# Performance work log

Hardware: AMD Instinct MI355X
Metric: run time of the kernel (lower is better)

The kernel has to match this reference:

```python
import jax, jax.numpy as jnp
import numpy as np

N = 50000   # nodes
E = 640000  # edges per outer layer
D = 128     # in_channels == num_hidden_channels
H = 4       # attention heads
C = D // H  # per-head dim = 32
BS = 1024   # batch_size for output slice
LN_EPS = 1e-12


def setup_inputs() -> dict:
    key = jax.random.key(0)
    ks = jax.random.split(key, 16)
    w = lambda k, shape: (jax.random.normal(k, shape, dtype=jnp.float32) * 0.05)
    return {
        "embs": jax.random.normal(ks[0], (N, D), dtype=jnp.float32),
        # GATv2 conv 0 (shared lin_l == lin_r since share_weights=True)
        "w0": w(ks[1], (D, H * C)),
        "b0": w(ks[2], (H * C,)),
        "att0": w(ks[3], (H, C)),
        "bias0": w(ks[4], (H * C,)),
        # GATv2 conv 1
        "w1": w(ks[5], (D, H * C)),
        "b1": w(ks[6], (H * C,)),
        "att1": w(ks[7], (H, C)),
        "bias1": w(ks[8], (H * C,)),
        # output head: Linear(D, D) + LayerNorm(D)
        "wout": w(ks[9], (D, D)),
        "bout": w(ks[10], (D,)),
        "gamma": jnp.ones((D,), dtype=jnp.float32),
        "beta": jnp.zeros((D,), dtype=jnp.float32),
        # graph structure (row 0 = source j, row 1 = target i, PyG convention)
        "edge_index0": jax.random.randint(ks[11], (2, E), 0, N, dtype=jnp.int32),
        "edge_index1": jax.random.randint(ks[12], (2, E), 0, N, dtype=jnp.int32),
        "batch_size": BS,
    }


def gatv2_conv(x, edge_index, w, b, att, bias):
    """PyG GATv2Conv: share_weights=True, add_self_loops=False, concat=True,
    negative_slope=0.2, edge_attr=None, eval mode (no attention dropout)."""
    xl = (x @ w + b).reshape(-1, H, C)          # [N, H, C]; x_l == x_r
    src, dst = edge_index[0], edge_index[1]
    xj = xl[src]                                # messages  [E, H, C]
    e = jax.nn.leaky_relu(xl[dst] + xj, negative_slope=0.2)
    alpha = jnp.einsum("ehc,hc->eh", e, att)    # [E, H]
    # segment softmax over incoming edges of each target node
    amax = jax.ops.segment_max(alpha, dst, num_segments=N)
    alpha = jnp.exp(alpha - amax[dst])
    denom = jax.ops.segment_sum(alpha, dst, num_segments=N)
    alpha = alpha / denom[dst]
    out = jax.ops.segment_sum(alpha[:, :, None] * xj, dst, num_segments=N)
    return out.reshape(-1, H * C) + bias        # [N, H*C]


def reference(embs, w0, b0, att0, bias0, w1, b1, att1, bias1,
              wout, bout, gamma, beta, edge_index0, edge_index1, batch_size):
    x = gatv2_conv(embs, edge_index0, w0, b0, att0, bias0)
    x = jax.nn.gelu(x, approximate=False)       # nn.GELU default (dropout is eval no-op)
    x = gatv2_conv(x, edge_index1, w1, b1, att1, bias1)
    # layernorm_output head on first batch_size nodes
    y = x[:batch_size] @ wout + bout
    mu = jnp.mean(y, axis=-1, keepdims=True)
    var = jnp.mean(jnp.square(y - mu), axis=-1, keepdims=True)
    return (y - mu) * jax.lax.rsqrt(var + LN_EPS) * gamma + beta
```

## Files before the change

kernel.cpp:

```cpp
#include <hip/hip_runtime.h>
#include <math.h>

#define DD 128
#define SLOT 64

typedef short bf16x8 __attribute__((ext_vector_type(8)));
typedef float f32x4  __attribute__((ext_vector_type(4)));

__device__ __forceinline__ unsigned bf16rne(float f) {
    unsigned u = __float_as_uint(f);
    return (u + 0x7FFFu + ((u >> 16) & 1u)) >> 16;
}
__device__ __forceinline__ float2 bf2f(unsigned u) {
    float2 r;
    r.x = __uint_as_float(u << 16);
    r.y = __uint_as_float(u & 0xFFFF0000u);
    return r;
}
__device__ __forceinline__ float gelu1(float v) {
    return 0.5f * v * (1.f + erff(v * 0.70710678118654752f));
}

__global__ __launch_bounds__(256) void k_mark(const int* __restrict__ src1,
                                              const int* __restrict__ dst1,
                                              int E1, int BS,
                                              unsigned* __restrict__ mb,
                                              const float* __restrict__ w0,
                                              const float* __restrict__ w1,
                                              unsigned short* __restrict__ wp0,
                                              unsigned short* __restrict__ wp1) {
    int idx = blockIdx.x * 256 + threadIdx.x;
    if (idx < 2 * DD * DD) {
        const float* w = (idx < DD * DD) ? w0 : w1;
        unsigned short* wp = (idx < DD * DD) ? wp0 : wp1;
        int i = idx & (DD * DD - 1);
        int k = i >> 7, c = i & 127;
        int nt = c >> 4, ks = k >> 5;
        int lane = (c & 15) | (((k >> 3) & 3) << 4);
        wp[(((nt * 4 + ks) * 64) + lane) * 8 + (k & 7)] =
            (unsigned short)bf16rne(w[k * DD + c]);
    }
    int base = blockIdx.x * 1024 + threadIdx.x;
    #pragma unroll
    for (int j = 0; j < 4; ++j) {
        int e = base + j * 256;
        if (e < E1) {
            int d = dst1[e];
            if (d < BS) {
                int s = src1[e];
                atomicOr(&mb[s >> 5], 1u << (s & 31));
            }
        }
    }
    int g = blockIdx.x * 256 + threadIdx.x;
    if (g < BS) atomicOr(&mb[g >> 5], 1u << (g & 31));
}

__device__ __forceinline__ void mfma_linear_rows(
        const float* __restrict__ x, const unsigned short* __restrict__ wp,
        const float* __restrict__ b, unsigned* __restrict__ xl,
        int rIn, int rowValid, int rbaseOut, int nrowsOut, int apply_gelu) {
    int lane = threadIdx.x & 63;
    int c = lane & 15, g = lane >> 4;
    f32x4 acc[8];
    #pragma unroll
    for (int nt = 0; nt < 8; ++nt) {
        float bb = b[nt * 16 + c];
        acc[nt] = (f32x4){bb, bb, bb, bb};
    }
    const bf16x8* wv = (const bf16x8*)wp;
    for (int ks = 0; ks < 4; ++ks) {
        float xr[8];
        if (rowValid) {
            const float4* xp = (const float4*)&x[(size_t)rIn * DD + ks * 32 + g * 8];
            *(float4*)&xr[0] = xp[0];
            *(float4*)&xr[4] = xp[1];
            if (apply_gelu) {
                #pragma unroll
                for (int j = 0; j < 8; ++j) xr[j] = gelu1(xr[j]);
            }
        } else {
            #pragma unroll
            for (int j = 0; j < 8; ++j) xr[j] = 0.f;
        }
        union { unsigned u[4]; bf16x8 v; } af;
        #pragma unroll
        for (int j = 0; j < 4; ++j)
            af.u[j] = bf16rne(xr[2 * j]) | (bf16rne(xr[2 * j + 1]) << 16);
        #pragma unroll
        for (int nt = 0; nt < 8; ++nt) {
            bf16x8 bv = wv[(nt * 4 + ks) * 64 + lane];
            acc[nt] = __builtin_amdgcn_mfma_f32_16x16x32_bf16(af.v, bv, acc[nt], 0, 0, 0);
        }
    }
    int g4 = g * 4;
    #pragma unroll
    for (int nt = 0; nt < 8; ++nt) {
        #pragma unroll
        for (int reg = 0; reg < 4; ++reg) {
            unsigned u = bf16rne(acc[nt][reg]);
            unsigned up = (unsigned)__shfl_xor((int)u, 1, 64);
            int row = rbaseOut + g4 + reg;
            if (!(c & 1) && row < nrowsOut)
                xl[(size_t)row * 64 + (nt * 16 + c) / 2] = u | (up << 16);
        }
    }
}

__global__ __launch_bounds__(256) void k_hflin(
        const float* __restrict__ x, const unsigned short* __restrict__ wp,
        const float* __restrict__ b, unsigned* __restrict__ y, int nrows,
        int gLin, int gH0, int gH1,
        const int* __restrict__ src0, const int* __restrict__ dst0, int E0,
        const int* __restrict__ src1, const int* __restrict__ dst1, int E1,
        int BS, const unsigned* __restrict__ mb, int* __restrict__ cnt,
        int* __restrict__ ssrc, int N,
        int W, int* __restrict__ mex, int* __restrict__ mbsum) {
    if (blockIdx.x >= gLin) {
        int role = blockIdx.x - gLin;
        if (role < gH0) {
            int base = role * 1024 + threadIdx.x;
            #pragma unroll
            for (int j = 0; j < 4; ++j) {
                int e = base + j * 256;
                if (e < E0) {
                    int d = dst0[e];
                    if ((mb[d >> 5] >> (d & 31)) & 1u) {
                        int r = atomicAdd(&cnt[d], 1);
                        if (r < SLOT) ssrc[(size_t)d * SLOT + r] = src0[e];
                    }
                }
            }
        } else if (role < gH0 + gH1) {
            int base = (role - gH0) * 1024 + threadIdx.x;
            #pragma unroll
            for (int j = 0; j < 4; ++j) {
                int e = base + j * 256;
                if (e < E1) {
                    int d = dst1[e];
                    if (d < BS) {
                        int r = atomicAdd(&cnt[N + d], 1);
                        if (r < SLOT) ssrc[(size_t)(N + d) * SLOT + r] = src1[e];
                    }
                }
            }
        } else {
            __shared__ int s[256];
            int idx = (role - gH0 - gH1) * 256 + threadIdx.x;
            int v = (idx < W) ? __popc(mb[idx]) : 0;
            s[threadIdx.x] = v;
            __syncthreads();
            for (int o = 1; o < 256; o <<= 1) {
                int t = (threadIdx.x >= o) ? s[threadIdx.x - o] : 0;
                __syncthreads();
                s[threadIdx.x] += t;
                __syncthreads();
            }
            if (idx < W) mex[idx] = s[threadIdx.x] - v;
            if (threadIdx.x == 255) mbsum[role - gH0 - gH1] = s[255];
        }
        return;
    }
    int wave = threadIdx.x >> 6;
    int rb = blockIdx.x * 64 + wave * 16;
    int rIn = rb + ((threadIdx.x & 63) & 15);
    mfma_linear_rows(x, wp, b, y, rIn, rIn < nrows, rb, nrows, 0);
}

__global__ __launch_bounds__(256) void k_aggL(const unsigned* __restrict__ xl,
                                              const int* __restrict__ cnt,
                                              const int* __restrict__ ssrc,
                                              const float* __restrict__ att,
                                              const float* __restrict__ bias,
                                              float* __restrict__ out,
                                              const unsigned* __restrict__ mb,
                                              int n, int gMs, int W,
                                              const int* __restrict__ mex,
                                              const int* __restrict__ mbsum,
                                              int* __restrict__ livelist,
                                              int* __restrict__ nLive) {
    if (blockIdx.x < gMs) {
        int pre = 0;
        for (int i = 0; i < (int)blockIdx.x; ++i) pre += mbsum[i];
        int idx = blockIdx.x * 256 + threadIdx.x;
        if (idx < W) {
            unsigned word = mb[idx];
            int base = mex[idx] + pre;
            unsigned wt = word;
            while (wt) {
                int bit = __ffs(wt) - 1;
                livelist[base + __popc(word & ((1u << bit) - 1u))] = idx * 32 + bit;
                wt &= wt - 1;
            }
            if (idx == W - 1) *nLive = base + __popc(word);
        }
        return;
    }
    int node = __builtin_amdgcn_readfirstlane((blockIdx.x - gMs) * 4 +
                                              (threadIdx.x >> 6));
    if (node >= n) return;
    if (!((mb[node >> 5] >> (node & 31)) & 1u)) return;
    int lane = threadIdx.x & 63;
    float2 attv = *(const float2*)&att[lane * 2];
    float2 xd = bf2f(xl[(size_t)node * 64 + lane]);
    int rs  = node * SLOT;
    int deg = cnt[node];
    deg = deg > SLOT ? SLOT : deg;

    float m = -3.4e38f, den = 0.f, accx = 0.f, accy = 0.f;
    int sA = (deg > 0) ? ssrc[rs] : 0;
    int sB = (deg > 1) ? ssrc[rs + 1] : 0;
    unsigned uA = xl[(size_t)sA * 64 + lane];
    unsigned uB = xl[(size_t)sB * 64 + lane];

    int k = 0;
    for (; k + 1 < deg; k += 2) {
        int sC = (k + 2 < deg) ? ssrc[rs + k + 2] : 0;
        int sD = (k + 3 < deg) ? ssrc[rs + k + 3] : 0;
        unsigned uC = xl[(size_t)sC * 64 + lane];
        unsigned uD = xl[(size_t)sD * 64 + lane];
        float2 vA = bf2f(uA), vB = bf2f(uB);

        float tx = xd.x + vA.x, ty = xd.y + vA.y;
        tx = tx > 0.f ? tx : 0.2f * tx;
        ty = ty > 0.f ? ty : 0.2f * ty;
        float l0 = tx * attv.x + ty * attv.y;
        tx = xd.x + vB.x; ty = xd.y + vB.y;
        tx = tx > 0.f ? tx : 0.2f * tx;
        ty = ty > 0.f ? ty : 0.2f * ty;
        float l1 = tx * attv.x + ty * attv.y;
        #pragma unroll
        for (int o = 8; o; o >>= 1) {
            l0 += __shfl_xor(l0, o, 64);
            l1 += __shfl_xor(l1, o, 64);
        }
        float mn = fmaxf(fmaxf(m, l0), l1);
        float corr = __expf(m - mn);
        float w0 = __expf(l0 - mn);
        float w1 = __expf(l1 - mn);
        den  = den  * corr + w0 + w1;
        accx = accx * corr + w0 * vA.x + w1 * vB.x;
        accy = accy * corr + w0 * vA.y + w1 * vB.y;
        m = mn;
        sA = sC; sB = sD; uA = uC; uB = uD;
    }
    if (k < deg) {
        float2 vA = bf2f(uA);
        float tx = xd.x + vA.x, ty = xd.y + vA.y;
        tx = tx > 0.f ? tx : 0.2f * tx;
        ty = ty > 0.f ? ty : 0.2f * ty;
        float l0 = tx * attv.x + ty * attv.y;
        #pragma unroll
        for (int o = 8; o; o >>= 1) l0 += __shfl_xor(l0, o, 64);
        float mn = fmaxf(m, l0);
        float corr = __expf(m - mn);
        float w0 = __expf(l0 - mn);
        den  = den  * corr + w0;
        accx = accx * corr + w0 * vA.x;
        accy = accy * corr + w0 * vA.y;
    }

    float inv = (deg > 0) ? 1.f / den : 0.f;
    float2 o2;
    o2.x = accx * inv + bias[lane * 2];
    o2.y = accy * inv + bias[lane * 2 + 1];
    *(float2*)&out[(size_t)node * DD + lane * 2] = o2;
}

__global__ __launch_bounds__(256) void k_linC(const float* __restrict__ x,
                                              const unsigned short* __restrict__ wp,
                                              const float* __restrict__ b,
                                              unsigned* __restrict__ y,
                                              const int* __restrict__ livelist,
                                              const int* __restrict__ nLive) {
    int nL = *nLive;
    int wave = threadIdx.x >> 6;
    int lb = blockIdx.x * 64 + wave * 16;
    if (blockIdx.x * 64 >= nL) return;
    int lane = threadIdx.x & 63;
    int liIn = lb + (lane & 15);
    int rIn = (liIn < nL) ? livelist[liIn] : 0;

    int c = lane & 15, g = lane >> 4;
    f32x4 acc[8];
    #pragma unroll
    for (int nt = 0; nt < 8; ++nt) {
        float bb = b[nt * 16 + c];
        acc[nt] = (f32x4){bb, bb, bb, bb};
    }
    const bf16x8* wv = (const bf16x8*)wp;
    for (int ks = 0; ks < 4; ++ks) {
        float xr[8];
        if (liIn < nL) {
            const float4* xp = (const float4*)&x[(size_t)rIn * DD + ks * 32 + g * 8];
            *(float4*)&xr[0] = xp[0];
            *(float4*)&xr[4] = xp[1];
            #pragma unroll
            for (int j = 0; j < 8; ++j) xr[j] = gelu1(xr[j]);
        } else {
            #pragma unroll
            for (int j = 0; j < 8; ++j) xr[j] = 0.f;
        }
        union { unsigned u[4]; bf16x8 v; } af;
        #pragma unroll
        for (int j = 0; j < 4; ++j)
            af.u[j] = bf16rne(xr[2 * j]) | (bf16rne(xr[2 * j + 1]) << 16);
        #pragma unroll
        for (int nt = 0; nt < 8; ++nt) {
            bf16x8 bv = wv[(nt * 4 + ks) * 64 + lane];
            acc[nt] = __builtin_amdgcn_mfma_f32_16x16x32_bf16(af.v, bv, acc[nt], 0, 0, 0);
        }
    }
    int g4 = g * 4;
    #pragma unroll
    for (int reg = 0; reg < 4; ++reg) {
        int liOut = lb + g4 + reg;
        int row = (liOut < nL) ? livelist[liOut] : -1;
        #pragma unroll
        for (int nt = 0; nt < 8; ++nt) {
            unsigned u = bf16rne(acc[nt][reg]);
            unsigned up = (unsigned)__shfl_xor((int)u, 1, 64);
            if (!(c & 1) && row >= 0)
                y[(size_t)row * 64 + (nt * 16 + c) / 2] = u | (up << 16);
        }
    }
}

__global__ __launch_bounds__(256) void k_agg1head(
        const unsigned* __restrict__ xl,
        const int* __restrict__ cnt, const int* __restrict__ ssrc,
        const float* __restrict__ att, const float* __restrict__ bias,
        const float* __restrict__ wout, const float* __restrict__ bout,
        const float* __restrict__ gamma, const float* __restrict__ beta,
        float* __restrict__ yout, int N, int BS) {
    __shared__ float xrow[4][DD];
    int wid  = threadIdx.x >> 6;
    int lane = threadIdx.x & 63;
    int node = blockIdx.x * 4 + wid;
    if (node >= BS) return;
    float2 attv = *(const float2*)&att[lane * 2];
    float2 xd = bf2f(xl[(size_t)node * 64 + lane]);
    int key = N + node;
    int rs  = key * SLOT;
    int deg = cnt[key];
    deg = deg > SLOT ? SLOT : deg;

    float m = -3.4e38f, den = 0.f, accx = 0.f, accy = 0.f;
    int sA = (deg > 0) ? ssrc[rs] : 0;
    int sB = (deg > 1) ? ssrc[rs + 1] : 0;
    unsigned uA = xl[(size_t)sA * 64 + lane];
    unsigned uB = xl[(size_t)sB * 64 + lane];

    int k = 0;
    for (; k + 1 < deg; k += 2) {
        int sC = (k + 2 < deg) ? ssrc[rs + k + 2] : 0;
        int sD = (k + 3 < deg) ? ssrc[rs + k + 3] : 0;
        unsigned uC = xl[(size_t)sC * 64 + lane];
        unsigned uD = xl[(size_t)sD * 64 + lane];
        float2 vA = bf2f(uA), vB = bf2f(uB);
        float tx = xd.x + vA.x, ty = xd.y + vA.y;
        tx = tx > 0.f ? tx : 0.2f * tx;
        ty = ty > 0.f ? ty : 0.2f * ty;
        float l0 = tx * attv.x + ty * attv.y;
        tx = xd.x + vB.x; ty = xd.y + vB.y;
        tx = tx > 0.f ? tx : 0.2f * tx;
        ty = ty > 0.f ? ty : 0.2f * ty;
        float l1 = tx * attv.x + ty * attv.y;
        #pragma unroll
        for (int o = 8; o; o >>= 1) {
            l0 += __shfl_xor(l0, o, 64);
            l1 += __shfl_xor(l1, o, 64);
        }
        float mn = fmaxf(fmaxf(m, l0), l1);
        float corr = __expf(m - mn);
        float w0 = __expf(l0 - mn);
        float w1 = __expf(l1 - mn);
        den  = den  * corr + w0 + w1;
        accx = accx * corr + w0 * vA.x + w1 * vB.x;
        accy = accy * corr + w0 * vA.y + w1 * vB.y;
        m = mn;
        sA = sC; sB = sD; uA = uC; uB = uD;
    }
    if (k < deg) {
        float2 vA = bf2f(uA);
        float tx = xd.x + vA.x, ty = xd.y + vA.y;
        tx = tx > 0.f ? tx : 0.2f * tx;
        ty = ty > 0.f ? ty : 0.2f * ty;
        float l0 = tx * attv.x + ty * attv.y;
        #pragma unroll
        for (int o = 8; o; o >>= 1) l0 += __shfl_xor(l0, o, 64);
        float mn = fmaxf(m, l0);
        float corr = __expf(m - mn);
        float w0 = __expf(l0 - mn);
        den  = den  * corr + w0;
        accx = accx * corr + w0 * vA.x;
        accy = accy * corr + w0 * vA.y;
    }

    float inv = (deg > 0) ? 1.f / den : 0.f;
    float2 o2;
    o2.x = accx * inv + bias[lane * 2];
    o2.y = accy * inv + bias[lane * 2 + 1];

    xrow[wid][lane * 2]     = o2.x;
    xrow[wid][lane * 2 + 1] = o2.y;
    float2 acc2 = *(const float2*)&bout[lane * 2];
    __syncthreads();
    #pragma unroll 4
    for (int kk = 0; kk < DD; ++kk) {
        float xv = xrow[wid][kk];
        float2 wv2 = *(const float2*)&wout[(size_t)kk * DD + lane * 2];
        acc2.x += xv * wv2.x;
        acc2.y += xv * wv2.y;
    }
    float s = acc2.x + acc2.y;
    #pragma unroll
    for (int o = 32; o; o >>= 1) s += __shfl_xor(s, o, 64);
    float mean = s * (1.f / 128.f);
    float dx = acc2.x - mean, dy = acc2.y - mean;
    float s2 = dx * dx + dy * dy;
    #pragma unroll
    for (int o = 32; o; o >>= 1) s2 += __shfl_xor(s2, o, 64);
    float rstd = rsqrtf(s2 * (1.f / 128.f) + 1e-12f);
    float2 g2 = *(const float2*)&gamma[lane * 2];
    float2 b2 = *(const float2*)&beta[lane * 2];
    float2 yo;
    yo.x = dx * rstd * g2.x + b2.x;
    yo.y = dy * rstd * g2.y + b2.y;
    *(float2*)&yout[(size_t)node * DD + lane * 2] = yo;
}

extern "C" void kernel_launch(void* const* d_in, const int* in_sizes, int n_in,
                              void* d_out, int out_size, void* d_ws, size_t ws_size,
                              hipStream_t stream) {
    const float* embs  = (const float*)d_in[0];
    const float* w0    = (const float*)d_in[1];
    const float* b0    = (const float*)d_in[2];
    const float* att0  = (const float*)d_in[3];
    const float* bias0 = (const float*)d_in[4];
    const float* w1    = (const float*)d_in[5];
    const float* b1    = (const float*)d_in[6];
    const float* att1  = (const float*)d_in[7];
    const float* bias1 = (const float*)d_in[8];
    const float* wout  = (const float*)d_in[9];
    const float* bout  = (const float*)d_in[10];
    const float* gamma = (const float*)d_in[11];
    const float* beta  = (const float*)d_in[12];
    const int* ei0 = (const int*)d_in[13];
    const int* ei1 = (const int*)d_in[14];

    int N  = in_sizes[0] / DD;
    int E0 = in_sizes[13] / 2;
    int E1 = in_sizes[14] / 2;
    int BS = out_size / DD;
    int n2 = N + BS;
    int W  = (N + 31) / 32;

    unsigned* xl   = (unsigned*)d_ws;
    float* out     = (float*)(xl + (size_t)N * 64);
    int* ssrc      = (int*)(out + (size_t)N * DD);
    int* cnt       = ssrc + (size_t)n2 * SLOT;
    unsigned* mb   = (unsigned*)(cnt + n2);
    int* mex       = (int*)(mb + W + 32);
    int* mbsum     = mex + W;
    int* livelist  = mbsum + 32;
    int* nLive     = livelist + N;
    unsigned short* wp0 = (unsigned short*)
        (((uintptr_t)(nLive + 1) + 15) & ~(uintptr_t)15);
    unsigned short* wp1 = wp0 + DD * DD;

    int gH0  = (E0 + 1023) / 1024;
    int gH1  = (E1 + 1023) / 1024;
    int gLin = (N + 63) / 64;
    int gMs  = (W + 255) / 256;

    hipMemsetAsync(cnt, 0, ((size_t)n2 + W + 32) * sizeof(int), stream);
    k_mark<<<gH1, 256, 0, stream>>>(ei1, ei1 + E1, E1, BS, mb, w0, w1, wp0, wp1);
    k_hflin<<<gLin + gH0 + gH1 + gMs, 256, 0, stream>>>(
        embs, wp0, b0, xl, N, gLin, gH0, gH1,
        ei0, ei0 + E0, E0, ei1, ei1 + E1, E1, BS,
        mb, cnt, ssrc, N, W, mex, mbsum);
    k_aggL<<<gMs + (N + 3) / 4, 256, 0, stream>>>(
        xl, cnt, ssrc, att0, bias0, out, mb, N, gMs, W,
        mex, mbsum, livelist, nLive);
    k_linC<<<gLin, 256, 0, stream>>>(out, wp1, b1, xl, livelist, nLive);
    k_agg1head<<<(BS + 3) / 4, 256, 0, stream>>>(
        xl, cnt, ssrc, att1, bias1,
        wout, bout, gamma, beta, (float*)d_out, N, BS);
}
```

Baseline: 94.58 us.

## Build live-node list via atomics in mark pass and stage weights in LDS

Live nodes are now appended to a compact list during the marking pass, using the old value returned by atomicOr, and the layer-1 CSR bucketing moves into that same kernel. This removes the popcount prefix-scan and list compaction stages. The aggregation kernel now launches over the live list instead of testing every node against the bitmask. Both MFMA linear kernels copy the packed bf16 weights into shared memory once per block, and the memset is replaced by a small zeroing kernel. In exchange, the live-list order becomes nondeterministic and all threads contend on a single global atomic counter.

```diff
diff --git a/kernel.cpp b/kernel.cpp
--- a/kernel.cpp
+++ b/kernel.cpp
@@ -21,10 +21,19 @@
     return 0.5f * v * (1.f + erff(v * 0.70710678118654752f));
 }
 
+__global__ __launch_bounds__(256) void k_zero(int* __restrict__ p, int T) {
+    int stride = gridDim.x * 256;
+    for (int i = blockIdx.x * 256 + threadIdx.x; i < T; i += stride) p[i] = 0;
+}
+
 __global__ __launch_bounds__(256) void k_mark(const int* __restrict__ src1,
                                               const int* __restrict__ dst1,
                                               int E1, int BS,
                                               unsigned* __restrict__ mb,
+                                              int* __restrict__ livelist,
+                                              int* __restrict__ nLive,
+                                              int* __restrict__ cnt,
+                                              int* __restrict__ ssrc, int N,
                                               const float* __restrict__ w0,
                                               const float* __restrict__ w1,
                                               unsigned short* __restrict__ wp0,
@@ -48,37 +57,73 @@
             int d = dst1[e];
             if (d < BS) {
                 int s = src1[e];
-                atomicOr(&mb[s >> 5], 1u << (s & 31));
+                int r = atomicAdd(&cnt[N + d], 1);
+                if (r < SLOT) ssrc[(size_t)(N + d) * SLOT + r] = s;
+                unsigned old = atomicOr(&mb[s >> 5], 1u << (s & 31));
+                if (!((old >> (s & 31)) & 1u))
+                    livelist[atomicAdd(nLive, 1)] = s;
             }
         }
     }
     int g = blockIdx.x * 256 + threadIdx.x;
-    if (g < BS) atomicOr(&mb[g >> 5], 1u << (g & 31));
-}
-
-__device__ __forceinline__ void mfma_linear_rows(
+    if (g < BS) {
+        unsigned old = atomicOr(&mb[g >> 5], 1u << (g & 31));
+        if (!((old >> (g & 31)) & 1u))
+            livelist[atomicAdd(nLive, 1)] = g;
+    }
+}
+
+__global__ __launch_bounds__(256) void k_hflin(
         const float* __restrict__ x, const unsigned short* __restrict__ wp,
-        const float* __restrict__ b, unsigned* __restrict__ xl,
-        int rIn, int rowValid, int rbaseOut, int nrowsOut, int apply_gelu) {
+        const float* __restrict__ b, unsigned* __restrict__ y, int nrows,
+        int gLin,
+        const int* __restrict__ src0, const int* __restrict__ dst0, int E0,
+        const unsigned* __restrict__ mb, int* __restrict__ cnt,
+        int* __restrict__ ssrc) {
+    __shared__ bf16x8 wl[2048];
+
+    if (blockIdx.x >= gLin) {
+        int role = blockIdx.x - gLin;
+        int base = role * 1024 + threadIdx.x;
+        #pragma unroll
+        for (int j = 0; j < 4; ++j) {
+            int e = base + j * 256;
+            if (e < E0) {
+                int d = dst0[e];
+                if ((mb[d >> 5] >> (d & 31)) & 1u) {
+                    int r = atomicAdd(&cnt[d], 1);
+                    if (r < SLOT) ssrc[(size_t)d * SLOT + r] = src0[e];
+                }
+            }
+        }
+        return;
+    }
+
+    const bf16x8* wg = (const bf16x8*)wp;
+    #pragma unroll
+    for (int i = 0; i < 8; ++i)
+        wl[threadIdx.x + i * 256] = wg[threadIdx.x + i * 256];
+    __syncthreads();
+
+    int wave = threadIdx.x >> 6;
+    int rb = blockIdx.x * 64 + wave * 16;
     int lane = threadIdx.x & 63;
     int c = lane & 15, g = lane >> 4;
+    int rIn = rb + c;
+    int rowValid = rIn < nrows;
+
     f32x4 acc[8];
     #pragma unroll
     for (int nt = 0; nt < 8; ++nt) {
         float bb = b[nt * 16 + c];
         acc[nt] = (f32x4){bb, bb, bb, bb};
     }
-    const bf16x8* wv = (const bf16x8*)wp;
     for (int ks = 0; ks < 4; ++ks) {
         float xr[8];
         if (rowValid) {
             const float4* xp = (const float4*)&x[(size_t)rIn * DD + ks * 32 + g * 8];
             *(float4*)&xr[0] = xp[0];
             *(float4*)&xr[4] = xp[1];
-            if (apply_gelu) {
-                #pragma unroll
-                for (int j = 0; j < 8; ++j) xr[j] = gelu1(xr[j]);
-            }
         } else {
             #pragma unroll
             for (int j = 0; j < 8; ++j) xr[j] = 0.f;
@@ -89,7 +134,7 @@
             af.u[j] = bf16rne(xr[2 * j]) | (bf16rne(xr[2 * j + 1]) << 16);
         #pragma unroll
         for (int nt = 0; nt < 8; ++nt) {
-            bf16x8 bv = wv[(nt * 4 + ks) * 64 + lane];
+            bf16x8 bv = wl[(nt * 4 + ks) * 64 + lane];
             acc[nt] = __builtin_amdgcn_mfma_f32_16x16x32_bf16(af.v, bv, acc[nt], 0, 0, 0);
         }
     }
@@ -100,71 +145,11 @@
         for (int reg = 0; reg < 4; ++reg) {
             unsigned u = bf16rne(acc[nt][reg]);
             unsigned up = (unsigned)__shfl_xor((int)u, 1, 64);
-            int row = rbaseOut + g4 + reg;
-            if (!(c & 1) && row < nrowsOut)
-                xl[(size_t)row * 64 + (nt * 16 + c) / 2] = u | (up << 16);
-        }
-    }
-}
-
-__global__ __launch_bounds__(256) void k_hflin(
-        const float* __restrict__ x, const unsigned short* __restrict__ wp,
-        const float* __restrict__ b, unsigned* __restrict__ y, int nrows,
-        int gLin, int gH0, int gH1,
-        const int* __restrict__ src0, const int* __restrict__ dst0, int E0,
-        const int* __restrict__ src1, const int* __restrict__ dst1, int E1,
-        int BS, const unsigned* __restrict__ mb, int* __restrict__ cnt,
-        int* __restrict__ ssrc, int N,
-        int W, int* __restrict__ mex, int* __restrict__ mbsum) {
-    if (blockIdx.x >= gLin) {
-        int role = blockIdx.x - gLin;
-        if (role < gH0) {
-            int base = role * 1024 + threadIdx.x;
-            #pragma unroll
-            for (int j = 0; j < 4; ++j) {
-                int e = base + j * 256;
-                if (e < E0) {
-                    int d = dst0[e];
-                    if ((mb[d >> 5] >> (d & 31)) & 1u) {
-                        int r = atomicAdd(&cnt[d], 1);
-                        if (r < SLOT) ssrc[(size_t)d * SLOT + r] = src0[e];
-                    }
-                }
-            }
-        } else if (role < gH0 + gH1) {
-            int base = (role - gH0) * 1024 + threadIdx.x;
-            #pragma unroll
-            for (int j = 0; j < 4; ++j) {
-                int e = base + j * 256;
-                if (e < E1) {
-                    int d = dst1[e];
-                    if (d < BS) {
-                        int r = atomicAdd(&cnt[N + d], 1);
-                        if (r < SLOT) ssrc[(size_t)(N + d) * SLOT + r] = src1[e];
-                    }
-                }
-            }
-        } else {
-            __shared__ int s[256];
-            int idx = (role - gH0 - gH1) * 256 + threadIdx.x;
-            int v = (idx < W) ? __popc(mb[idx]) : 0;
-            s[threadIdx.x] = v;
-            __syncthreads();
-            for (int o = 1; o < 256; o <<= 1) {
-                int t = (threadIdx.x >= o) ? s[threadIdx.x - o] : 0;
-                __syncthreads();
-                s[threadIdx.x] += t;
-                __syncthreads();
-            }
-            if (idx < W) mex[idx] = s[threadIdx.x] - v;
-            if (threadIdx.x == 255) mbsum[role - gH0 - gH1] = s[255];
-        }
-        return;
-    }
-    int wave = threadIdx.x >> 6;
-    int rb = blockIdx.x * 64 + wave * 16;
-    int rIn = rb + ((threadIdx.x & 63) & 15);
-    mfma_linear_rows(x, wp, b, y, rIn, rIn < nrows, rb, nrows, 0);
+            int row = rb + g4 + reg;
+            if (!(c & 1) && row < nrows)
+                y[(size_t)row * 64 + (nt * 16 + c) / 2] = u | (up << 16);
+        }
+    }
 }
 
 __global__ __launch_bounds__(256) void k_aggL(const unsigned* __restrict__ xl,
@@ -173,33 +158,11 @@
                                               const float* __restrict__ att,
                                               const float* __restrict__ bias,
                                               float* __restrict__ out,
-                                              const unsigned* __restrict__ mb,
-                                              int n, int gMs, int W,
-                                              const int* __restrict__ mex,
-                                              const int* __restrict__ mbsum,
-                                              int* __restrict__ livelist,
-                                              int* __restrict__ nLive) {
-    if (blockIdx.x < gMs) {
-        int pre = 0;
-        for (int i = 0; i < (int)blockIdx.x; ++i) pre += mbsum[i];
-        int idx = blockIdx.x * 256 + threadIdx.x;
-        if (idx < W) {
-            unsigned word = mb[idx];
-            int base = mex[idx] + pre;
-            unsigned wt = word;
-            while (wt) {
-                int bit = __ffs(wt) - 1;
-                livelist[base + __popc(word & ((1u << bit) - 1u))] = idx * 32 + bit;
-                wt &= wt - 1;
-            }
-            if (idx == W - 1) *nLive = base + __popc(word);
-        }
-        return;
-    }
-    int node = __builtin_amdgcn_readfirstlane((blockIdx.x - gMs) * 4 +
-                                              (threadIdx.x >> 6));
-    if (node >= n) return;
-    if (!((mb[node >> 5] >> (node & 31)) & 1u)) return;
+                                              const int* __restrict__ livelist,
+                                              const int* __restrict__ nLive) {
+    int li = blockIdx.x * 4 + (threadIdx.x >> 6);
+    if (li >= *nLive) return;
+    int node = __builtin_amdgcn_readfirstlane(livelist[li]);
     int lane = threadIdx.x & 63;
     float2 attv = *(const float2*)&att[lane * 2];
     float2 xd = bf2f(xl[(size_t)node * 64 + lane]);
@@ -273,22 +236,29 @@
                                               unsigned* __restrict__ y,
                                               const int* __restrict__ livelist,
                                               const int* __restrict__ nLive) {
+    __shared__ bf16x8 wl[2048];
     int nL = *nLive;
+    if (blockIdx.x * 64 >= nL) return;
+
+    const bf16x8* wg = (const bf16x8*)wp;
+    #pragma unroll
+    for (int i = 0; i < 8; ++i)
+        wl[threadIdx.x + i * 256] = wg[threadIdx.x + i * 256];
+    __syncthreads();
+
     int wave = threadIdx.x >> 6;
     int lb = blockIdx.x * 64 + wave * 16;
-    if (blockIdx.x * 64 >= nL) return;
     int lane = threadIdx.x & 63;
-    int liIn = lb + (lane & 15);
+    int c = lane & 15, g = lane >> 4;
+    int liIn = lb + c;
     int rIn = (liIn < nL) ? livelist[liIn] : 0;
 
-    int c = lane & 15, g = lane >> 4;
     f32x4 acc[8];
     #pragma unroll
     for (int nt = 0; nt < 8; ++nt) {
         float bb = b[nt * 16 + c];
         acc[nt] = (f32x4){bb, bb, bb, bb};
     }
-    const bf16x8* wv = (const bf16x8*)wp;
     for (int ks = 0; ks < 4; ++ks) {
         float xr[8];
         if (liIn < nL) {
@@ -307,7 +277,7 @@
             af.u[j] = bf16rne(xr[2 * j]) | (bf16rne(xr[2 * j + 1]) << 16);
         #pragma unroll
         for (int nt = 0; nt < 8; ++nt) {
-            bf16x8 bv = wv[(nt * 4 + ks) * 64 + lane];
+            bf16x8 bv = wl[(nt * 4 + ks) * 64 + lane];
             acc[nt] = __builtin_amdgcn_mfma_f32_16x16x32_bf16(af.v, bv, acc[nt], 0, 0, 0);
         }
     }
@@ -461,28 +431,24 @@
     int* ssrc      = (int*)(out + (size_t)N * DD);
     int* cnt       = ssrc + (size_t)n2 * SLOT;
     unsigned* mb   = (unsigned*)(cnt + n2);
-    int* mex       = (int*)(mb + W + 32);
-    int* mbsum     = mex + W;
-    int* livelist  = mbsum + 32;
-    int* nLive     = livelist + N;
+    int* nLive     = (int*)(mb + W + 32);
+    int* livelist  = nLive + 1;
     unsigned short* wp0 = (unsigned short*)
-        (((uintptr_t)(nLive + 1) + 15) & ~(uintptr_t)15);
+        (((uintptr_t)(livelist + N) + 15) & ~(uintptr_t)15);
     unsigned short* wp1 = wp0 + DD * DD;
 
     int gH0  = (E0 + 1023) / 1024;
     int gH1  = (E1 + 1023) / 1024;
     int gLin = (N + 63) / 64;
-    int gMs  = (W + 255) / 256;
-
-    hipMemsetAsync(cnt, 0, ((size_t)n2 + W + 32) * sizeof(int), stream);
-    k_mark<<<gH1, 256, 0, stream>>>(ei1, ei1 + E1, E1, BS, mb, w0, w1, wp0, wp1);
-    k_hflin<<<gLin + gH0 + gH1 + gMs, 256, 0, stream>>>(
-        embs, wp0, b0, xl, N, gLin, gH0, gH1,
-        ei0, ei0 + E0, E0, ei1, ei1 + E1, E1, BS,
-        mb, cnt, ssrc, N, W, mex, mbsum);
-    k_aggL<<<gMs + (N + 3) / 4, 256, 0, stream>>>(
-        xl, cnt, ssrc, att0, bias0, out, mb, N, gMs, W,
-        mex, mbsum, livelist, nLive);
+    int Tz   = n2 + W + 32 + 1;
+
+    k_zero<<<64, 256, 0, stream>>>(cnt, Tz);
+    k_mark<<<gH1, 256, 0, stream>>>(ei1, ei1 + E1, E1, BS, mb, livelist, nLive,
+                                    cnt, ssrc, N, w0, w1, wp0, wp1);
+    k_hflin<<<gLin + gH0, 256, 0, stream>>>(
+        embs, wp0, b0, xl, N, gLin, ei0, ei0 + E0, E0, mb, cnt, ssrc);
+    k_aggL<<<(N + 3) / 4, 256, 0, stream>>>(xl, cnt, ssrc, att0, bias0, out,
+                                            livelist, nLive);
     k_linC<<<gLin, 256, 0, stream>>>(out, wp1, b1, xl, livelist, nLive);
     k_agg1head<<<(BS + 3) / 4, 256, 0, stream>>>(
         xl, cnt, ssrc, att1, bias1,
```

New measurement: 147.7 us. 1.56x slower.
